# Kernel tuning notes

Measured on AMD Instinct MI355X. Metric: run time of the kernel, lower is better.

The kernel has to match this reference:

```python
import jax, jax.numpy as jnp
import numpy as np

TEMP = 5.0

def _conv2d_same(x, w):
    # x [Q, Cin, H, W], w [Cout, Cin, 3, 3]
    return jax.lax.conv_general_dilated(x, w, (1, 1), 'SAME',
        dimension_numbers=('NCHW', 'OIHW', 'NCHW'))

def _sep_conv4d(x, w_hw, w_uv):
    # Separable 4D conv: 3x3 conv over (Hb,Wb) + 3x3 conv over (Hm,Wm), summed.
    # x [Q, Cin, U, V, H, W]
    Q, Cin, U, V, H, W = x.shape
    Cout = w_hw.shape[0]
    x_hw = x.transpose(0, 2, 3, 1, 4, 5).reshape(Q * U * V, Cin, H, W)
    y_hw = _conv2d_same(x_hw, w_hw).reshape(Q, U, V, Cout, H, W).transpose(0, 3, 1, 2, 4, 5)
    x_uv = x.transpose(0, 4, 5, 1, 2, 3).reshape(Q * H * W, Cin, U, V)
    y_uv = _conv2d_same(x_uv, w_uv).reshape(Q, H, W, Cout, U, V).transpose(0, 3, 4, 5, 1, 2)
    return y_hw + y_uv

def _gaussian_normalize(x, axis, eps=1e-5):
    m = jnp.mean(x, axis=axis, keepdims=True)
    v = jnp.var(x, axis=axis, keepdims=True, ddof=1)  # torch.var is unbiased
    return (x - m) / jnp.sqrt(v + eps)

def _embed(x, w1x1, bn_scale, bn_bias):
    # 1x1 conv + (folded) BN affine + ReLU + channel L2-normalize (F.normalize eps=1e-8)
    y = jnp.einsum('bchw,oc->bohw', x, w1x1)
    y = y * bn_scale[None, :, None, None] + bn_bias[None, :, None, None]
    y = jax.nn.relu(y)
    n = jnp.sqrt(jnp.sum(y * y, axis=1, keepdims=True))
    return y / jnp.maximum(n, 1e-8)

def _forward(feat_b, feat_m, w1x1, bn_scale, bn_bias, w1_hw, w1_uv, w2_hw, w2_uv, W_fc, b_fc):
    feat_m = jax.lax.stop_gradient(feat_m)  # encoder(memory).detach()
    # channel mean shift (only for attention path)
    fbs = feat_b - jnp.mean(feat_b, axis=1, keepdims=True)
    fms = feat_m - jnp.mean(feat_m, axis=1, keepdims=True)
    fb = _embed(fbs, w1x1, bn_scale, bn_bias)  # [B,R,Hb,Wb]
    fm = _embed(fms, w1x1, bn_scale, bn_bias)  # [N,R,Hm,Wm]
    corr = jnp.einsum('bchw,ncij->bnijhw', fb, fm)  # [B,N,Hm,Wm,Hb,Wb]
    B, N, Hm, Wm, Hb, Wb = corr.shape
    x = corr.reshape(B * N, 1, Hm, Wm, Hb, Wb)
    x = jax.nn.relu(_sep_conv4d(x, w1_hw, w1_uv))
    x = _sep_conv4d(x, w2_hw, w2_uv)
    corr = x.reshape(B, N, Hm, Wm, Hb, Wb)
    # attention over memory spatial positions
    cm = corr.reshape(B, N, Hm * Wm, Hb, Wb)
    cm = jax.nn.softmax(_gaussian_normalize(cm, 2) / TEMP, axis=2)
    attn_memory = cm.reshape(B, N, Hm, Wm, Hb, Wb).sum(axis=(4, 5))  # [B,N,Hm,Wm]
    # attention over batch spatial positions (computed in torch forward too)
    cb = corr.reshape(B, N, Hm, Wm, Hb * Wb)
    cb = jax.nn.softmax(_gaussian_normalize(cb, 4) / TEMP, axis=4)
    attn_batch = cb.reshape(B, N, Hm, Wm, Hb, Wb).sum(axis=(2, 3))  # [B,N,Hb,Wb]
    att_mem = jnp.einsum('bnhw,nchw->bnc', attn_memory, feat_m) / (Hm * Wm)  # [B,N,C]
    _att_bat = jnp.einsum('bnhw,bchw->bnc', attn_batch, feat_b) / (Hb * Wb)  # unused by logits
    encoder_output = jnp.mean(feat_b, axis=(-1, -2))  # [B,C]
    # BatchMemoryWrapLayer: cosine-similarity content attention over memory, concat + linear
    e_n = jnp.maximum(jnp.linalg.norm(encoder_output, axis=-1, keepdims=True), 1e-8)
    m_n = jnp.maximum(jnp.linalg.norm(att_mem, axis=-1), 1e-8)
    sim = jnp.einsum('bc,bnc->bn', encoder_output, att_mem) / (e_n * m_n)
    w = jax.nn.softmax(sim, axis=1)
    mem_vec = jnp.einsum('bn,bnc->bc', w, att_mem)
    logits = jnp.concatenate([encoder_output, mem_vec], axis=-1) @ W_fc + b_fc
    return logits

def setup_inputs() -> dict:
    key = jax.random.key(0)
    ks = jax.random.split(key, 9)
    feat_b = jax.random.normal(ks[0], (8, 640, 10, 10), jnp.float32)
    feat_m = jax.random.normal(ks[1], (50, 640, 10, 10), jnp.float32)
    w1x1 = jax.random.normal(ks[2], (64, 640), jnp.float32) * 0.05
    bn_scale = jnp.ones((64,), jnp.float32)
    bn_bias = jnp.zeros((64,), jnp.float32)
    w1_hw = jax.random.normal(ks[3], (16, 1, 3, 3), jnp.float32) * 0.2
    w1_uv = jax.random.normal(ks[4], (16, 1, 3, 3), jnp.float32) * 0.2
    w2_hw = jax.random.normal(ks[5], (1, 16, 3, 3), jnp.float32) * 0.2
    w2_uv = jax.random.normal(ks[6], (1, 16, 3, 3), jnp.float32) * 0.2
    W_fc = jax.random.normal(ks[7], (1280, 1000), jnp.float32) * 0.02
    b_fc = jnp.zeros((1000,), jnp.float32)
    return dict(feat_b=feat_b, feat_m=feat_m, w1x1=w1x1, bn_scale=bn_scale, bn_bias=bn_bias,
                w1_hw=w1_hw, w1_uv=w1_uv, w2_hw=w2_hw, w2_uv=w2_uv, W_fc=W_fc, b_fc=b_fc)

def reference(feat_b, feat_m, w1x1, bn_scale, bn_bias, w1_hw, w1_uv, w2_hw, w2_uv, W_fc, b_fc):
    return _forward(feat_b, feat_m, w1x1, bn_scale, bn_bias, w1_hw, w1_uv, w2_hw, w2_uv, W_fc, b_fc)
```

## Files before the change

kernel.cpp:

```cpp
#include <hip/hip_runtime.h>

#define WS_WT    0
#define WS_WSUM  40960
#define WS_FB    41024
#define WS_FM    92224
#define WS_ATTN  412224
#define WS_AM    452224
#define WS_ENC   708224
#define WS_MV    713344

__global__ void k_prep(const float* __restrict__ w1x1, float* __restrict__ wT2,
                       float* __restrict__ wsum) {
  if (blockIdx.x < 160) {
    int idx = blockIdx.x * 256 + threadIdx.x;
    int o = idx / 640, c = idx % 640;
    wT2[((c >> 2) * 64 + o) * 4 + (c & 3)] = w1x1[idx];
  } else if (threadIdx.x < 64) {
    int o = threadIdx.x;
    float s = 0.f;
    for (int c = 0; c < 640; ++c) s += w1x1[o * 640 + c];
    wsum[o] = s;
  }
}

__global__ void k_embed(const float* __restrict__ fbg, const float* __restrict__ fmg,
                        const float* __restrict__ wT2, const float* __restrict__ wsum,
                        const float* __restrict__ bns, const float* __restrict__ bnb,
                        float* __restrict__ fb, float* __restrict__ fm,
                        float* __restrict__ enc) {
  int lane = threadIdx.x;
  if (blockIdx.x >= 580) {
    int b = blockIdx.x - 580;
    for (int c = lane; c < 640; c += 64) {
      const float4* fp = (const float4*)(fbg + (b * 640 + c) * 100);
      float s = 0.f;
#pragma unroll
      for (int t4 = 0; t4 < 25; ++t4) { float4 v = fp[t4]; s += v.x + v.y + v.z + v.w; }
      enc[b * 640 + c] = s * 0.01f;
    }
    return;
  }
  int pos0 = blockIdx.x * 10;
  const float* src; float* dst; int hw0;
  if (pos0 < 800) { int img = pos0 / 100; hw0 = pos0 % 100; src = fbg + img * 64000; dst = fb + pos0 * 64; }
  else { int p = pos0 - 800; int img = p / 100; hw0 = p % 100; src = fmg + img * 64000; dst = fm + p * 64; }

  __shared__ float xs[10][640];
  float lsum[10];
#pragma unroll
  for (int p = 0; p < 10; ++p) lsum[p] = 0.f;
  for (int i = 0; i < 10; ++i) {
    int c = lane + i * 64;
    const float* sp = src + c * 100 + hw0;
#pragma unroll
    for (int p = 0; p < 10; p += 2) {
      float2 v = *(const float2*)(sp + p);
      xs[p][c] = v.x; xs[p + 1][c] = v.y;
      lsum[p] += v.x; lsum[p + 1] += v.y;
    }
  }
  float mean[10];
#pragma unroll
  for (int p = 0; p < 10; ++p) {
    float s = lsum[p];
    for (int off = 32; off; off >>= 1) s += __shfl_down(s, off);
    mean[p] = __shfl(s, 0) * (1.f / 640.f);
  }
  __syncthreads();
  float acc[10];
#pragma unroll
  for (int p = 0; p < 10; ++p) acc[p] = 0.f;
  for (int c4 = 0; c4 < 160; ++c4) {
    float4 w4 = *(const float4*)(wT2 + (c4 * 64 + lane) * 4);
#pragma unroll
    for (int p = 0; p < 10; ++p) {
      float4 x4 = *(const float4*)(&xs[p][c4 * 4]);
      acc[p] += w4.x * x4.x + w4.y * x4.y + w4.z * x4.z + w4.w * x4.w;
    }
  }
  float wsl = wsum[lane], sc = bns[lane], bi = bnb[lane];
#pragma unroll
  for (int p = 0; p < 10; ++p) {
    float y = (acc[p] - mean[p] * wsl) * sc + bi;
    y = fmaxf(y, 0.f);
    float sq = y * y;
    for (int off = 32; off; off >>= 1) sq += __shfl_down(sq, off);
    float nrm = sqrtf(__shfl(sq, 0));
    dst[p * 64 + lane] = y / fmaxf(nrm, 1e-8f);
  }
}


#define ROFF(r) (12 + (r) * 12)

#define LOAD_ROW12Z(DST, BASE, ROW, OK) {                                   \
    int _o = (OK) ? ROFF(ROW) : 0;                                          \
    float4 _a = *(const float4*)((BASE) + _o);                              \
    float4 _b = *(const float4*)((BASE) + _o + 4);                          \
    float4 _c = *(const float4*)((BASE) + _o + 8);                          \
    DST[0]=_a.x; DST[1]=_a.y; DST[2]=_a.z; DST[3]=_a.w;                     \
    DST[4]=_b.x; DST[5]=_b.y; DST[6]=_b.z; DST[7]=_b.w;                     \
    DST[8]=_c.x; DST[9]=_c.y; }

#define HW_TAPS(OUT, ROW, W0, W1, W2) {                                     \
    _Pragma("unroll") for (int w = 1; w < 10; ++w) OUT[w] += (W0)*ROW[w-1]; \
    _Pragma("unroll") for (int w = 0; w < 10; ++w) OUT[w] += (W1)*ROW[w];   \
    _Pragma("unroll") for (int w = 0; w < 9;  ++w) OUT[w] += (W2)*ROW[w+1]; }

#define UV_TAPS(ACCARR, ROW, WARR) {                                        \
    _Pragma("unroll") for (int i = 0; i < 2; ++i) {                         \
      _Pragma("unroll") for (int j = 0; j < 2; ++j) {                       \
        int du = uu - 1 - i, dv = vv - 1 - j;                               \
        if (du >= -1 && du <= 1 && dv >= -1 && dv <= 1) {                   \
          float wgt = WARR[(du+1)*3 + (dv+1)];                              \
          _Pragma("unroll") for (int w = 0; w < 10; ++w)                    \
            ACCARR[i*2+j][w] += wgt * ROW[w];                               \
        } } } }

__global__ __launch_bounds__(256, 1) void k_mid(
    const float* __restrict__ fb, const float* __restrict__ fm,
    const float* __restrict__ w1h_g, const float* __restrict__ w1u_g,
    const float* __restrict__ w2h_g, const float* __restrict__ w2u_g,
    float* __restrict__ attn)
{
  __shared__ float xs[12012];
  __shared__ float c1[12012];
  __shared__ float rcps[100];
  const int tid = threadIdx.x, q = blockIdx.x;
  const int b = q / 50, n = q % 50;

  const bool act = tid < 250;
  const int pu = tid / 50, prem = tid % 50, pv = prem / 10, h = prem % 10;
  const int u0 = pu * 2, v0 = pv * 2;
  const int ij0 = u0 * 10 + v0;

  if (tid < 12) xs[tid] = 0.f;

  for (int i = tid; i < 1600; i += 256) {
    int hw = i >> 4, c4 = (i & 15) << 2;
    *(float4*)(c1 + hw * 68 + c4) = *(const float4*)(fb + b * 6400 + hw * 64 + c4);
  }
  __syncthreads();

#pragma unroll 1
  for (int pass = 0; pass < 2; ++pass) {
    if (act) {
      int ijb = ij0 + pass * 10;
      float fmA[64], fmB[64];
      const float* p0 = fm + n * 6400 + ijb * 64;
#pragma unroll
      for (int c4 = 0; c4 < 16; ++c4) {
        float4 vA = *(const float4*)(p0 + c4 * 4);
        float4 vB = *(const float4*)(p0 + 64 + c4 * 4);
        fmA[c4*4+0]=vA.x; fmA[c4*4+1]=vA.y; fmA[c4*4+2]=vA.z; fmA[c4*4+3]=vA.w;
        fmB[c4*4+0]=vB.x; fmB[c4*4+1]=vB.y; fmB[c4*4+2]=vB.z; fmB[c4*4+3]=vB.w;
      }
      float a0[10], a1[10];
#pragma unroll
      for (int w = 0; w < 10; ++w) {
        const float* rw = c1 + (h * 10 + w) * 68;
        float s0 = 0.f, s1 = 0.f;
#pragma unroll
        for (int c4 = 0; c4 < 16; ++c4) {
          float4 v = *(const float4*)(rw + c4 * 4);
          s0 += v.x*fmA[4*c4] + v.y*fmA[4*c4+1] + v.z*fmA[4*c4+2] + v.w*fmA[4*c4+3];
          s1 += v.x*fmB[4*c4] + v.y*fmB[4*c4+1] + v.z*fmB[4*c4+2] + v.w*fmB[4*c4+3];
        }
        a0[w] = s0; a1[w] = s1;
      }
      float* r0p = xs + ROFF(ijb * 10 + h);
      *(float4*)(r0p)     = make_float4(a0[0],a0[1],a0[2],a0[3]);
      *(float4*)(r0p + 4) = make_float4(a0[4],a0[5],a0[6],a0[7]);
      *(float4*)(r0p + 8) = make_float4(a0[8],a0[9],0.f,0.f);
      float* r1p = xs + ROFF((ijb + 1) * 10 + h);
      *(float4*)(r1p)     = make_float4(a1[0],a1[1],a1[2],a1[3]);
      *(float4*)(r1p + 4) = make_float4(a1[4],a1[5],a1[6],a1[7]);
      *(float4*)(r1p + 8) = make_float4(a1[8],a1[9],0.f,0.f);
    }
  }
  __syncthreads();

  if (tid < 12) c1[tid] = 0.f;

  float X[4][4][10];
  float acc[4][10];
  if (act) {
#pragma unroll
    for (int uu = 0; uu < 4; ++uu)
#pragma unroll
      for (int vv = 0; vv < 4; ++vv) {
        if (uu >= 1 && uu <= 2 && vv >= 1 && vv <= 2) continue;
        int up = u0 - 1 + uu, vp = v0 - 1 + vv;
        bool ok = (up >= 0) && (up < 10) && (vp >= 0) && (vp < 10);
        LOAD_ROW12Z(X[uu][vv], xs, (up * 10 + vp) * 10 + h, ok);
      }
#pragma unroll
    for (int oi = 0; oi < 4; ++oi)
#pragma unroll
      for (int w = 0; w < 10; ++w) acc[oi][w] = 0.f;
  }

  for (int k = 0; k < 16; ++k) {
    float wA[9], wB[9];
#pragma unroll
    for (int t = 0; t < 9; ++t) { wA[t] = w1h_g[k * 9 + t]; wB[t] = w1u_g[k * 9 + t]; }
    if (act) {
      float O4[4][10];
#pragma unroll
      for (int i = 0; i < 2; ++i)
#pragma unroll
        for (int j = 0; j < 2; ++j)
          LOAD_ROW12Z(O4[i*2+j], xs, ((u0+i)*10 + (v0+j))*10 + h, true);
#pragma unroll
      for (int i = 0; i < 2; ++i)
#pragma unroll
        for (int j = 0; j < 2; ++j) {
          int oi = i*2+j;
          float o[10];
#pragma unroll
          for (int w = 0; w < 10; ++w) o[w] = 0.f;
          HW_TAPS(o, O4[oi], wA[3], wA[4], wA[5]);
          {
            float R[10];
            LOAD_ROW12Z(R, xs, ((u0+i)*10 + (v0+j))*10 + (h-1), h > 0);
            HW_TAPS(o, R, wA[0], wA[1], wA[2]);
            LOAD_ROW12Z(R, xs, ((u0+i)*10 + (v0+j))*10 + (h+1), h < 9);
            HW_TAPS(o, R, wA[6], wA[7], wA[8]);
          }
#pragma unroll
          for (int du = -1; du <= 1; ++du)
#pragma unroll
            for (int dv = -1; dv <= 1; ++dv) {
              int ii = i + du, jj = j + dv;
              float wgt = wB[(du+1)*3 + (dv+1)];
              if (ii >= 0 && ii <= 1 && jj >= 0 && jj <= 1) {
#pragma unroll
                for (int w = 0; w < 10; ++w) o[w] += wgt * O4[ii*2+jj][w];
              } else {
#pragma unroll
                for (int w = 0; w < 10; ++w) o[w] += wgt * X[1+ii][1+jj][w];
              }
            }
          float* cp = c1 + ROFF(((u0+i)*10 + (v0+j))*10 + h);
          *(float4*)(cp)     = make_float4(fmaxf(o[0],0.f), fmaxf(o[1],0.f), fmaxf(o[2],0.f), fmaxf(o[3],0.f));
          *(float4*)(cp + 4) = make_float4(fmaxf(o[4],0.f), fmaxf(o[5],0.f), fmaxf(o[6],0.f), fmaxf(o[7],0.f));
          *(float4*)(cp + 8) = make_float4(fmaxf(o[8],0.f), fmaxf(o[9],0.f), 0.f, 0.f);
        }
    }
    __syncthreads();
#pragma unroll
    for (int t = 0; t < 9; ++t) { wA[t] = w2h_g[k * 9 + t]; wB[t] = w2u_g[k * 9 + t]; }
    if (act) {
#pragma unroll
      for (int uu = 0; uu < 4; ++uu)
#pragma unroll
        for (int vv = 0; vv < 4; ++vv) {
          float R[10];
          int up = u0 - 1 + uu, vp = v0 - 1 + vv;
          bool ok = (up >= 0) && (up < 10) && (vp >= 0) && (vp < 10);
          LOAD_ROW12Z(R, c1, (up*10 + vp)*10 + h, ok);
          UV_TAPS(acc, R, wB);
          if (uu >= 1 && uu <= 2 && vv >= 1 && vv <= 2) {
            int oi = (uu-1)*2 + (vv-1);
            HW_TAPS(acc[oi], R, wA[3], wA[4], wA[5]);
          }
        }
#pragma unroll
      for (int i = 0; i < 2; ++i)
#pragma unroll
        for (int j = 0; j < 2; ++j) {
          int oi = i*2+j;
          float R[10];
          LOAD_ROW12Z(R, c1, ((u0+i)*10 + (v0+j))*10 + (h-1), h > 0);
          HW_TAPS(acc[oi], R, wA[0], wA[1], wA[2]);
          LOAD_ROW12Z(R, c1, ((u0+i)*10 + (v0+j))*10 + (h+1), h < 9);
          HW_TAPS(acc[oi], R, wA[6], wA[7], wA[8]);
        }
    }
    __syncthreads();
  }

  if (act) {
#pragma unroll
    for (int i = 0; i < 2; ++i)
#pragma unroll
      for (int j = 0; j < 2; ++j) {
        int ij = (u0 + i) * 10 + (v0 + j);
#pragma unroll
        for (int w = 0; w < 10; ++w) c1[(h*10 + w)*108 + ij] = acc[i*2+j][w];
      }
  }
  __syncthreads();
  if (tid < 100) {
    float* row = c1 + tid * 108;
    float s = 0.f;
#pragma unroll
    for (int t4 = 0; t4 < 25; ++t4) {
      float4 v = *(const float4*)(row + t4 * 4);
      s += v.x + v.y + v.z + v.w;
    }
    float mean = s * 0.01f;
    float vs = 0.f, mx = -1e30f;
#pragma unroll
    for (int t4 = 0; t4 < 25; ++t4) {
      float4 v = *(const float4*)(row + t4 * 4);
      float d0 = v.x-mean, d1 = v.y-mean, d2 = v.z-mean, d3 = v.w-mean;
      vs += d0*d0 + d1*d1 + d2*d2 + d3*d3;
      mx = fmaxf(mx, fmaxf(fmaxf(d0, d1), fmaxf(d2, d3)));
    }
    float inv = 1.f / (5.f * sqrtf(vs * (1.f / 99.f) + 1e-5f));
    float es = 0.f;
#pragma unroll
    for (int t4 = 0; t4 < 25; ++t4) {
      float4 v = *(const float4*)(row + t4 * 4);
      float4 e;
      e.x = expf((v.x - mean - mx) * inv);
      e.y = expf((v.y - mean - mx) * inv);
      e.z = expf((v.z - mean - mx) * inv);
      e.w = expf((v.w - mean - mx) * inv);
      es += e.x + e.y + e.z + e.w;
      *(float4*)(row + t4 * 4) = e;
    }
    rcps[tid] = 1.f / es;
  }
  __syncthreads();
  if (tid < 100) {
    float s = 0.f;
    for (int hw = 0; hw < 100; ++hw) s += c1[hw * 108 + tid] * rcps[hw];
    attn[q * 100 + tid] = s;
  }
}

__global__ void k_attmem(const float* __restrict__ attn, const float* __restrict__ fmg,
                         float* __restrict__ am) {
  int q = blockIdx.x, n = q % 50;
  __shared__ float a[100];
  if (threadIdx.x < 100) a[threadIdx.x] = attn[q * 100 + threadIdx.x];
  __syncthreads();
  for (int c = threadIdx.x; c < 640; c += 256) {
    const float4* fp = (const float4*)(fmg + (n * 640 + c) * 100);
    float s = 0.f;
#pragma unroll
    for (int t4 = 0; t4 < 25; ++t4) {
      float4 v = fp[t4];
      s += a[t4*4]*v.x + a[t4*4+1]*v.y + a[t4*4+2]*v.z + a[t4*4+3]*v.w;
    }
    am[q * 640 + c] = s * 0.01f;
  }
}

__global__ void k_final1(const float* __restrict__ enc, const float* __restrict__ am,
                         float* __restrict__ mv) {
  int b = blockIdx.x, tid = threadIdx.x;
  __shared__ float e[640];
  __shared__ float wsm[50];
  __shared__ float wred[4];
  for (int c = tid; c < 640; c += 256) e[c] = enc[b * 640 + c];
  __syncthreads();
  float ps = 0.f;
  for (int c = tid; c < 640; c += 256) { float x = e[c]; ps += x * x; }
  for (int off = 32; off; off >>= 1) ps += __shfl_down(ps, off);
  if ((tid & 63) == 0) wred[tid >> 6] = ps;
  __syncthreads();
  float en = fmaxf(sqrtf(wred[0] + wred[1] + wred[2] + wred[3]), 1e-8f);
  if (tid < 50) {
    const float* ap = am + (b * 50 + tid) * 640;
    float dot = 0.f, nn = 0.f;
    for (int c = 0; c < 640; ++c) { float x = ap[c]; dot += x * e[c]; nn += x * x; }
    wsm[tid] = dot / (en * fmaxf(sqrtf(nn), 1e-8f));
  }
  __syncthreads();
  if (tid == 0) {
    float mx = -1e30f;
    for (int n2 = 0; n2 < 50; ++n2) mx = fmaxf(mx, wsm[n2]);
    float es = 0.f;
    for (int n2 = 0; n2 < 50; ++n2) { float ex = expf(wsm[n2] - mx); wsm[n2] = ex; es += ex; }
    float rr = 1.f / es;
    for (int n2 = 0; n2 < 50; ++n2) wsm[n2] *= rr;
  }
  __syncthreads();
  for (int c = tid; c < 640; c += 256) {
    float s = 0.f;
    for (int n2 = 0; n2 < 50; ++n2) s += wsm[n2] * am[(b * 50 + n2) * 640 + c];
    mv[b * 640 + c] = s;
  }
}

__global__ void k_logits(const float* __restrict__ enc, const float* __restrict__ mv,
                         const float* __restrict__ Wfc, const float* __restrict__ bfc,
                         float* __restrict__ out) {
  int b = blockIdx.x >> 4, jc = blockIdx.x & 15;
  int t = threadIdx.x;
  __shared__ float cat[1280];
  for (int c = t; c < 640; c += 64) {
    cat[c] = enc[b * 640 + c];
    cat[640 + c] = mv[b * 640 + c];
  }
  __syncthreads();
  int j = jc * 64 + t;
  if (j < 1000) {
    float s0 = bfc[j], s1 = 0.f, s2 = 0.f, s3 = 0.f;
    for (int c = 0; c < 1280; c += 4) {
      s0 += cat[c]     * Wfc[c * 1000 + j];
      s1 += cat[c + 1] * Wfc[(c + 1) * 1000 + j];
      s2 += cat[c + 2] * Wfc[(c + 2) * 1000 + j];
      s3 += cat[c + 3] * Wfc[(c + 3) * 1000 + j];
    }
    out[b * 1000 + j] = (s0 + s1) + (s2 + s3);
  }
}

extern "C" void kernel_launch(void* const* d_in, const int* in_sizes, int n_in,
                              void* d_out, int out_size, void* d_ws, size_t ws_size,
                              hipStream_t stream) {
  const float* feat_b = (const float*)d_in[0];
  const float* feat_m = (const float*)d_in[1];
  const float* w1x1   = (const float*)d_in[2];
  const float* bns    = (const float*)d_in[3];
  const float* bnb    = (const float*)d_in[4];
  const float* w1h    = (const float*)d_in[5];
  const float* w1u    = (const float*)d_in[6];
  const float* w2h    = (const float*)d_in[7];
  const float* w2u    = (const float*)d_in[8];
  const float* Wfc    = (const float*)d_in[9];
  const float* bfc    = (const float*)d_in[10];
  float* ws = (float*)d_ws;
  float* wT2  = ws + WS_WT;   float* wsum = ws + WS_WSUM;
  float* fbW  = ws + WS_FB;   float* fmW  = ws + WS_FM;
  float* attn = ws + WS_ATTN; float* am   = ws + WS_AM;
  float* enc  = ws + WS_ENC;  float* mv   = ws + WS_MV;

  k_prep   <<<161, 256, 0, stream>>>(w1x1, wT2, wsum);
  k_embed  <<<588,  64, 0, stream>>>(feat_b, feat_m, wT2, wsum, bns, bnb, fbW, fmW, enc);
  k_mid    <<<400, 256, 0, stream>>>(fbW, fmW, w1h, w1u, w2h, w2u, attn);
  k_attmem <<<400, 256, 0, stream>>>(attn, feat_m, am);
  k_final1 <<<8,   256, 0, stream>>>(enc, am, mv);
  k_logits <<<128,  64, 0, stream>>>(enc, mv, Wfc, bfc, (float*)d_out);
}
```

Baseline: 322.6 us.

## Share memory-feature loads across batch in attmem and split final1 dot products

k_attmem now indexes blocks by memory item and channel tile rather than by (batch, memory) pair. Each feat_m row is loaded once and applied to all 8 batch attention vectors held in shared memory, with 4 threads per channel reduced by shuffles. The aim is to cut redundant global reads of feat_m, which were previously repeated for every batch element. k_final1 splits each 640-long cosine dot product across 4 threads with float4 loads and shuffle reduction, using 200 threads instead of 50 serial loops.

```diff
diff --git a/kernel.cpp b/kernel.cpp
--- a/kernel.cpp
+++ b/kernel.cpp
@@ -333,19 +333,37 @@
 
 __global__ void k_attmem(const float* __restrict__ attn, const float* __restrict__ fmg,
                          float* __restrict__ am) {
-  int q = blockIdx.x, n = q % 50;
-  __shared__ float a[100];
-  if (threadIdx.x < 100) a[threadIdx.x] = attn[q * 100 + threadIdx.x];
-  __syncthreads();
-  for (int c = threadIdx.x; c < 640; c += 256) {
-    const float4* fp = (const float4*)(fmg + (n * 640 + c) * 100);
-    float s = 0.f;
-#pragma unroll
-    for (int t4 = 0; t4 < 25; ++t4) {
-      float4 v = fp[t4];
-      s += a[t4*4]*v.x + a[t4*4+1]*v.y + a[t4*4+2]*v.z + a[t4*4+3]*v.w;
-    }
-    am[q * 640 + c] = s * 0.01f;
+  int n = blockIdx.x / 10, ct = blockIdx.x % 10;
+  int t = threadIdx.x;
+  __shared__ float a_s[800];
+  for (int i = t; i < 800; i += 256) {
+    int ij = i >> 3, bb = i & 7;
+    a_s[i] = attn[(bb * 50 + n) * 100 + ij];
+  }
+  __syncthreads();
+  int c = ct * 64 + (t >> 2), qq = t & 3;
+  const float* fp = fmg + (n * 640 + c) * 100;
+  float s[8];
+#pragma unroll
+  for (int bb = 0; bb < 8; ++bb) s[bb] = 0.f;
+#pragma unroll 5
+  for (int i = 0; i < 25; ++i) {
+    int ij = qq + 4 * i;
+    float v = fp[ij];
+    const float4* ap = (const float4*)(a_s + ij * 8);
+    float4 A0 = ap[0], A1 = ap[1];
+    s[0] += A0.x * v; s[1] += A0.y * v; s[2] += A0.z * v; s[3] += A0.w * v;
+    s[4] += A1.x * v; s[5] += A1.y * v; s[6] += A1.z * v; s[7] += A1.w * v;
+  }
+#pragma unroll
+  for (int bb = 0; bb < 8; ++bb) {
+    s[bb] += __shfl_xor(s[bb], 1);
+    s[bb] += __shfl_xor(s[bb], 2);
+  }
+  if (qq == 0) {
+#pragma unroll
+    for (int bb = 0; bb < 8; ++bb)
+      am[(bb * 50 + n) * 640 + c] = s[bb] * 0.01f;
   }
 }
 
@@ -363,11 +381,21 @@
   if ((tid & 63) == 0) wred[tid >> 6] = ps;
   __syncthreads();
   float en = fmaxf(sqrtf(wred[0] + wred[1] + wred[2] + wred[3]), 1e-8f);
-  if (tid < 50) {
-    const float* ap = am + (b * 50 + tid) * 640;
+  if (tid < 200) {
+    int n2 = tid >> 2, qq = tid & 3;
+    const float* ap = am + (b * 50 + n2) * 640 + qq * 160;
+    const float* ep = e + qq * 160;
     float dot = 0.f, nn = 0.f;
-    for (int c = 0; c < 640; ++c) { float x = ap[c]; dot += x * e[c]; nn += x * x; }
-    wsm[tid] = dot / (en * fmaxf(sqrtf(nn), 1e-8f));
+#pragma unroll 10
+    for (int c = 0; c < 160; c += 4) {
+      float4 x = *(const float4*)(ap + c);
+      float4 ee = *(const float4*)(ep + c);
+      dot += x.x * ee.x + x.y * ee.y + x.z * ee.z + x.w * ee.w;
+      nn  += x.x * x.x + x.y * x.y + x.z * x.z + x.w * x.w;
+    }
+    dot += __shfl_xor(dot, 1); dot += __shfl_xor(dot, 2);
+    nn  += __shfl_xor(nn, 1);  nn  += __shfl_xor(nn, 2);
+    if (qq == 0) wsm[n2] = dot / (en * fmaxf(sqrtf(nn), 1e-8f));
   }
   __syncthreads();
   if (tid == 0) {
@@ -433,7 +461,7 @@
   k_prep   <<<161, 256, 0, stream>>>(w1x1, wT2, wsum);
   k_embed  <<<588,  64, 0, stream>>>(feat_b, feat_m, wT2, wsum, bns, bnb, fbW, fmW, enc);
   k_mid    <<<400, 256, 0, stream>>>(fbW, fmW, w1h, w1u, w2h, w2u, attn);
-  k_attmem <<<400, 256, 0, stream>>>(attn, feat_m, am);
+  k_attmem <<<500, 256, 0, stream>>>(attn, feat_m, am);
   k_final1 <<<8,   256, 0, stream>>>(enc, am, mv);
   k_logits <<<128,  64, 0, stream>>>(enc, mv, Wfc, bfc, (float*)d_out);
 }
```

Measured after the change: 305.1 us. 1.06x faster.

## Fuse kernels: drop weight prep, merge attmem into mid, merge final stages

Applied to the files above, without the earlier changes.

Removes the weight-transpose prep kernel and has embed read w1x1 rows directly while accumulating the row sum on the fly. Folds the attention-weighted memory pooling into the tail of k_mid so attention weights stay in shared memory, and merges the final cosine-softmax and logits kernels into one 128-block kernel with the FC reduction split across four wavefronts. This cuts launches from six to three and drops intermediate global buffers. The cost is that k_finale recomputes the per-batch softmax and memory vector redundantly in all sixteen blocks, and embed's weight loads are no longer coalesced across lanes.

```diff
diff --git a/kernel.cpp b/kernel.cpp
--- a/kernel.cpp
+++ b/kernel.cpp
@@ -1,30 +1,12 @@
 #include <hip/hip_runtime.h>
 
-#define WS_WT    0
-#define WS_WSUM  40960
-#define WS_FB    41024
-#define WS_FM    92224
-#define WS_ATTN  412224
-#define WS_AM    452224
-#define WS_ENC   708224
-#define WS_MV    713344
-
-__global__ void k_prep(const float* __restrict__ w1x1, float* __restrict__ wT2,
-                       float* __restrict__ wsum) {
-  if (blockIdx.x < 160) {
-    int idx = blockIdx.x * 256 + threadIdx.x;
-    int o = idx / 640, c = idx % 640;
-    wT2[((c >> 2) * 64 + o) * 4 + (c & 3)] = w1x1[idx];
-  } else if (threadIdx.x < 64) {
-    int o = threadIdx.x;
-    float s = 0.f;
-    for (int c = 0; c < 640; ++c) s += w1x1[o * 640 + c];
-    wsum[o] = s;
-  }
-}
+#define WS_FB    0
+#define WS_FM    51200
+#define WS_AM    371200
+#define WS_ENC   627200
 
 __global__ void k_embed(const float* __restrict__ fbg, const float* __restrict__ fmg,
-                        const float* __restrict__ wT2, const float* __restrict__ wsum,
+                        const float* __restrict__ w1x1,
                         const float* __restrict__ bns, const float* __restrict__ bnb,
                         float* __restrict__ fb, float* __restrict__ fm,
                         float* __restrict__ enc) {
@@ -70,15 +52,18 @@
   float acc[10];
 #pragma unroll
   for (int p = 0; p < 10; ++p) acc[p] = 0.f;
+  float wsl = 0.f;
+  const float* wrow = w1x1 + lane * 640;
   for (int c4 = 0; c4 < 160; ++c4) {
-    float4 w4 = *(const float4*)(wT2 + (c4 * 64 + lane) * 4);
+    float4 w4 = *(const float4*)(wrow + c4 * 4);
+    wsl += w4.x + w4.y + w4.z + w4.w;
 #pragma unroll
     for (int p = 0; p < 10; ++p) {
       float4 x4 = *(const float4*)(&xs[p][c4 * 4]);
       acc[p] += w4.x * x4.x + w4.y * x4.y + w4.z * x4.z + w4.w * x4.w;
     }
   }
-  float wsl = wsum[lane], sc = bns[lane], bi = bnb[lane];
+  float sc = bns[lane], bi = bnb[lane];
 #pragma unroll
   for (int p = 0; p < 10; ++p) {
     float y = (acc[p] - mean[p] * wsl) * sc + bi;
@@ -121,11 +106,12 @@
     const float* __restrict__ fb, const float* __restrict__ fm,
     const float* __restrict__ w1h_g, const float* __restrict__ w1u_g,
     const float* __restrict__ w2h_g, const float* __restrict__ w2u_g,
-    float* __restrict__ attn)
+    const float* __restrict__ fmg, float* __restrict__ am)
 {
   __shared__ float xs[12012];
   __shared__ float c1[12012];
   __shared__ float rcps[100];
+  __shared__ float attnS[100];
   const int tid = threadIdx.x, q = blockIdx.x;
   const int b = q / 50, n = q % 50;
 
@@ -327,47 +313,55 @@
   if (tid < 100) {
     float s = 0.f;
     for (int hw = 0; hw < 100; ++hw) s += c1[hw * 108 + tid] * rcps[hw];
-    attn[q * 100 + tid] = s;
-  }
-}
-
-__global__ void k_attmem(const float* __restrict__ attn, const float* __restrict__ fmg,
-                         float* __restrict__ am) {
-  int q = blockIdx.x, n = q % 50;
-  __shared__ float a[100];
-  if (threadIdx.x < 100) a[threadIdx.x] = attn[q * 100 + threadIdx.x];
-  __syncthreads();
-  for (int c = threadIdx.x; c < 640; c += 256) {
-    const float4* fp = (const float4*)(fmg + (n * 640 + c) * 100);
+    attnS[tid] = s;
+  }
+  __syncthreads();
+
+  const float* fmn = fmg + n * 64000;
+  for (int c = tid; c < 640; c += 256) {
+    const float4* fp = (const float4*)(fmn + c * 100);
     float s = 0.f;
 #pragma unroll
     for (int t4 = 0; t4 < 25; ++t4) {
       float4 v = fp[t4];
-      s += a[t4*4]*v.x + a[t4*4+1]*v.y + a[t4*4+2]*v.z + a[t4*4+3]*v.w;
+      s += attnS[t4*4]*v.x + attnS[t4*4+1]*v.y + attnS[t4*4+2]*v.z + attnS[t4*4+3]*v.w;
     }
     am[q * 640 + c] = s * 0.01f;
   }
 }
 
-__global__ void k_final1(const float* __restrict__ enc, const float* __restrict__ am,
-                         float* __restrict__ mv) {
-  int b = blockIdx.x, tid = threadIdx.x;
-  __shared__ float e[640];
+__global__ void k_finale(const float* __restrict__ enc, const float* __restrict__ am,
+                         const float* __restrict__ Wfc, const float* __restrict__ bfc,
+                         float* __restrict__ out) {
+  int b = blockIdx.x >> 4, jt = blockIdx.x & 15;
+  int tid = threadIdx.x;
+  __shared__ float cat[1280];
   __shared__ float wsm[50];
   __shared__ float wred[4];
-  for (int c = tid; c < 640; c += 256) e[c] = enc[b * 640 + c];
+  __shared__ float part[4][64];
+  for (int c = tid; c < 640; c += 256) cat[c] = enc[b * 640 + c];
   __syncthreads();
   float ps = 0.f;
-  for (int c = tid; c < 640; c += 256) { float x = e[c]; ps += x * x; }
+  for (int c = tid; c < 640; c += 256) { float x = cat[c]; ps += x * x; }
   for (int off = 32; off; off >>= 1) ps += __shfl_down(ps, off);
   if ((tid & 63) == 0) wred[tid >> 6] = ps;
   __syncthreads();
   float en = fmaxf(sqrtf(wred[0] + wred[1] + wred[2] + wred[3]), 1e-8f);
-  if (tid < 50) {
-    const float* ap = am + (b * 50 + tid) * 640;
+  if (tid < 200) {
+    int n2 = tid >> 2, qq = tid & 3;
+    const float* ap = am + (b * 50 + n2) * 640 + qq * 160;
+    const float* ep = cat + qq * 160;
     float dot = 0.f, nn = 0.f;
-    for (int c = 0; c < 640; ++c) { float x = ap[c]; dot += x * e[c]; nn += x * x; }
-    wsm[tid] = dot / (en * fmaxf(sqrtf(nn), 1e-8f));
+#pragma unroll 10
+    for (int c = 0; c < 160; c += 4) {
+      float4 x = *(const float4*)(ap + c);
+      float4 ee = *(const float4*)(ep + c);
+      dot += x.x * ee.x + x.y * ee.y + x.z * ee.z + x.w * ee.w;
+      nn  += x.x * x.x + x.y * x.y + x.z * x.z + x.w * x.w;
+    }
+    dot += __shfl_xor(dot, 1); dot += __shfl_xor(dot, 2);
+    nn  += __shfl_xor(nn, 1);  nn  += __shfl_xor(nn, 2);
+    if (qq == 0) wsm[n2] = dot / (en * fmaxf(sqrtf(nn), 1e-8f));
   }
   __syncthreads();
   if (tid == 0) {
@@ -382,31 +376,26 @@
   for (int c = tid; c < 640; c += 256) {
     float s = 0.f;
     for (int n2 = 0; n2 < 50; ++n2) s += wsm[n2] * am[(b * 50 + n2) * 640 + c];
-    mv[b * 640 + c] = s;
-  }
-}
-
-__global__ void k_logits(const float* __restrict__ enc, const float* __restrict__ mv,
-                         const float* __restrict__ Wfc, const float* __restrict__ bfc,
-                         float* __restrict__ out) {
-  int b = blockIdx.x >> 4, jc = blockIdx.x & 15;
-  int t = threadIdx.x;
-  __shared__ float cat[1280];
-  for (int c = t; c < 640; c += 64) {
-    cat[c] = enc[b * 640 + c];
-    cat[640 + c] = mv[b * 640 + c];
-  }
-  __syncthreads();
-  int j = jc * 64 + t;
+    cat[640 + c] = s;
+  }
+  __syncthreads();
+  int w = tid >> 6, jl = tid & 63;
+  int j = jt * 64 + jl;
+  float s0 = 0.f, s1 = 0.f, s2 = 0.f, s3 = 0.f;
   if (j < 1000) {
-    float s0 = bfc[j], s1 = 0.f, s2 = 0.f, s3 = 0.f;
-    for (int c = 0; c < 1280; c += 4) {
-      s0 += cat[c]     * Wfc[c * 1000 + j];
-      s1 += cat[c + 1] * Wfc[(c + 1) * 1000 + j];
-      s2 += cat[c + 2] * Wfc[(c + 2) * 1000 + j];
-      s3 += cat[c + 3] * Wfc[(c + 3) * 1000 + j];
-    }
-    out[b * 1000 + j] = (s0 + s1) + (s2 + s3);
+    const float* wp = Wfc + j;
+    int c0 = w * 320;
+    for (int c = c0; c < c0 + 320; c += 4) {
+      s0 += cat[c]     * wp[c * 1000];
+      s1 += cat[c + 1] * wp[(c + 1) * 1000];
+      s2 += cat[c + 2] * wp[(c + 2) * 1000];
+      s3 += cat[c + 3] * wp[(c + 3) * 1000];
+    }
+  }
+  part[w][jl] = (s0 + s1) + (s2 + s3);
+  __syncthreads();
+  if (tid < 64 && j < 1000) {
+    out[b * 1000 + j] = bfc[j] + ((part[0][jl] + part[1][jl]) + (part[2][jl] + part[3][jl]));
   }
 }
 
@@ -425,15 +414,10 @@
   const float* Wfc    = (const float*)d_in[9];
   const float* bfc    = (const float*)d_in[10];
   float* ws = (float*)d_ws;
-  float* wT2  = ws + WS_WT;   float* wsum = ws + WS_WSUM;
-  float* fbW  = ws + WS_FB;   float* fmW  = ws + WS_FM;
-  float* attn = ws + WS_ATTN; float* am   = ws + WS_AM;
-  float* enc  = ws + WS_ENC;  float* mv   = ws + WS_MV;
-
-  k_prep   <<<161, 256, 0, stream>>>(w1x1, wT2, wsum);
-  k_embed  <<<588,  64, 0, stream>>>(feat_b, feat_m, wT2, wsum, bns, bnb, fbW, fmW, enc);
-  k_mid    <<<400, 256, 0, stream>>>(fbW, fmW, w1h, w1u, w2h, w2u, attn);
-  k_attmem <<<400, 256, 0, stream>>>(attn, feat_m, am);
-  k_final1 <<<8,   256, 0, stream>>>(enc, am, mv);
-  k_logits <<<128,  64, 0, stream>>>(enc, mv, Wfc, bfc, (float*)d_out);
+  float* fbW = ws + WS_FB;  float* fmW = ws + WS_FM;
+  float* am  = ws + WS_AM;  float* enc = ws + WS_ENC;
+
+  k_embed  <<<588,  64, 0, stream>>>(feat_b, feat_m, w1x1, bns, bnb, fbW, fmW, enc);
+  k_mid    <<<400, 256, 0, stream>>>(fbW, fmW, w1h, w1u, w2h, w2u, feat_m, am);
+  k_finale <<<128, 256, 0, stream>>>(enc, am, Wfc, bfc, (float*)d_out);
 }
```

Measured after the change: 266.7 us (median of 2 runs). 1.21x faster.
